# Kernel tuning notes

Measured on AMD Instinct MI355X. Metric: run time of the kernel, lower is better.

Reference implementation:

```python
import jax, jax.numpy as jnp
import numpy as np

BLOCK = 64  # quantization block size along in_features
IN, OUT, RANK, ALPHA = 4096, 4096, 16, 32
SCALING = ALPHA / RANK


def setup_inputs() -> dict:
    key = jax.random.key(0)
    ks = jax.random.split(key, 6)
    x = jax.random.normal(ks[0], (8, 1024, IN), dtype=jnp.float32)
    # int4 codes in [0, 15]; dequant subtracts 8 -> [-8, 7]
    qweight = jax.random.randint(ks[1], (OUT, IN), 0, 16, dtype=jnp.int32)
    # blockwise absmax-style scales, small positive
    scales = jax.random.uniform(ks[2], (OUT, IN // BLOCK), dtype=jnp.float32) * 0.02 + 1e-3
    bias = jax.random.normal(ks[3], (OUT,), dtype=jnp.float32) * 0.02
    lora_A = jax.random.normal(ks[4], (IN, RANK), dtype=jnp.float32) * 0.02
    lora_B = jnp.zeros((RANK, OUT), dtype=jnp.float32)
    return {"x": x, "qweight": qweight, "scales": scales, "bias": bias,
            "lora_A": lora_A, "lora_B": lora_B}


def _dequant(qweight, scales):
    # qweight: [out, in] int codes in [0,15]; scales: [out, in/BLOCK]
    out, in_f = qweight.shape
    q = (qweight.astype(jnp.float32) - 8.0).reshape(out, in_f // BLOCK, BLOCK)
    return (q * scales[:, :, None]).reshape(out, in_f)  # [out, in]


def reference(x, qweight, scales, bias, lora_A, lora_B):
    W = _dequant(qweight, scales)                      # [out, in]
    base = jnp.einsum('bsi,oi->bso', x, W) + bias      # quantized linear
    lora = jnp.einsum('bsr,ro->bso', jnp.einsum('bsi,ir->bsr', x, lora_A), lora_B)
    return base + lora * SCALING
```

## Files before the change

kernel.cpp:

```cpp
#include <hip/hip_runtime.h>
#include <hip/hip_bf16.h>

#define IN_F 4096
#define OUT_F 4096
#define M_TOK 8192
#define RANK 16

typedef __attribute__((ext_vector_type(4))) float f32x4;
typedef __attribute__((ext_vector_type(8))) short short8;

struct alignas(16) bf16x8_s { __hip_bfloat16 v[8]; };

#define CONV_BLOCKS 2048
#define CONV_ITERS (M_TOK * IN_F / (8 * 256 * CONV_BLOCKS))

__global__ __launch_bounds__(256) void conv_kernel(
    const float* __restrict__ x,
    __hip_bfloat16* __restrict__ xb) {
    size_t idx = (size_t)blockIdx.x * 256 + threadIdx.x;
    const size_t stride = (size_t)CONV_BLOCKS * 256;
#pragma unroll
    for (int it = 0; it < CONV_ITERS; ++it, idx += stride) {
        const size_t base = idx * 8;
        float4 v0 = *(const float4*)(x + base);
        float4 v1 = *(const float4*)(x + base + 4);
        bf16x8_s r;
        r.v[0] = __float2bfloat16(v0.x);
        r.v[1] = __float2bfloat16(v0.y);
        r.v[2] = __float2bfloat16(v0.z);
        r.v[3] = __float2bfloat16(v0.w);
        r.v[4] = __float2bfloat16(v1.x);
        r.v[5] = __float2bfloat16(v1.y);
        r.v[6] = __float2bfloat16(v1.z);
        r.v[7] = __float2bfloat16(v1.w);
        *(bf16x8_s*)(xb + base) = r;
    }
}

#define DEQ_BLOCKS 2048

__global__ __launch_bounds__(256) void deq_kernel(
    const int* __restrict__ q,
    const float* __restrict__ scales,
    const float* __restrict__ lA,
    const float* __restrict__ lB,
    __hip_bfloat16* __restrict__ W) {
    const int tid = threadIdx.x;
    const int bid = blockIdx.x;
    const int o0 = (bid >> 1) * 4;
    const int i0 = (bid & 1) * 2048 + tid * 8;

    float bw[16][4];
#pragma unroll
    for (int r = 0; r < 16; ++r)
#pragma unroll
        for (int oi = 0; oi < 4; ++oi)
            bw[r][oi] = 2.0f * lB[(size_t)r * OUT_F + o0 + oi];

    float fold[4][8];
#pragma unroll
    for (int e = 0; e < 8; ++e) {
        const float* ar = lA + (size_t)(i0 + e) * RANK;
        float4 a0 = *(const float4*)(ar + 0);
        float4 a1 = *(const float4*)(ar + 4);
        float4 a2 = *(const float4*)(ar + 8);
        float4 a3 = *(const float4*)(ar + 12);
#pragma unroll
        for (int oi = 0; oi < 4; ++oi) {
            float f = a0.x * bw[0][oi] + a0.y * bw[1][oi]
                    + a0.z * bw[2][oi] + a0.w * bw[3][oi]
                    + a1.x * bw[4][oi] + a1.y * bw[5][oi]
                    + a1.z * bw[6][oi] + a1.w * bw[7][oi]
                    + a2.x * bw[8][oi] + a2.y * bw[9][oi]
                    + a2.z * bw[10][oi] + a2.w * bw[11][oi]
                    + a3.x * bw[12][oi] + a3.y * bw[13][oi]
                    + a3.z * bw[14][oi] + a3.w * bw[15][oi];
            fold[oi][e] = f;
        }
    }

#pragma unroll
    for (int oi = 0; oi < 4; ++oi) {
        const int o = o0 + oi;
        const float s = scales[o * 64 + (i0 >> 6)];
        const int4* qp = (const int4*)(q + (size_t)o * IN_F + i0);
        int4 q0 = qp[0];
        int4 q1 = qp[1];
        bf16x8_s r;
        r.v[0] = __float2bfloat16(s * (float)(q0.x - 8) + fold[oi][0]);
        r.v[1] = __float2bfloat16(s * (float)(q0.y - 8) + fold[oi][1]);
        r.v[2] = __float2bfloat16(s * (float)(q0.z - 8) + fold[oi][2]);
        r.v[3] = __float2bfloat16(s * (float)(q0.w - 8) + fold[oi][3]);
        r.v[4] = __float2bfloat16(s * (float)(q1.x - 8) + fold[oi][4]);
        r.v[5] = __float2bfloat16(s * (float)(q1.y - 8) + fold[oi][5]);
        r.v[6] = __float2bfloat16(s * (float)(q1.z - 8) + fold[oi][6]);
        r.v[7] = __float2bfloat16(s * (float)(q1.w - 8) + fold[oi][7]);
        *(bf16x8_s*)(W + (size_t)o * IN_F + i0) = r;
    }
}

#define BK 64
#define NT (IN_F / BK)

__device__ __forceinline__ short8 ldfrag(const short* p, int half, int row, int gran) {
    return *(const short8*)(p + half * 8192 + row * 64 + ((gran ^ (row & 7)) * 8));
}

#define STAGE(LDSbuf, SRC, ROW0, K0)                                          \
    {                                                                         \
        _Pragma("unroll")                                                     \
        for (int j = 0; j < 2; ++j) {                                         \
            const __hip_bfloat16* g = (SRC) +                                 \
                (size_t)((ROW0) + j * 64 + wave * 8 + srow) * IN_F + (K0) + sgc; \
            __builtin_amdgcn_global_load_lds(                                 \
                (const __attribute__((address_space(1))) void*)g,             \
                (__attribute__((address_space(3))) void*)((LDSbuf) + (j * 64 + wave * 8) * 64), \
                16, 0, 0);                                                    \
        }                                                                     \
    }

#define PHASE(ABUF, BBUF, MH, KK, READB, STAGE_CODE, WAITCODE)                \
    {                                                                         \
        _Pragma("unroll") for (int f = 0; f < 4; ++f)                         \
            fa[f] = ldfrag(ABUF, MH, wm * 64 + f * 16 + fr, (KK) * 4 + fc);   \
        if (READB) {                                                          \
            _Pragma("unroll") for (int g2 = 0; g2 < 4; ++g2)                  \
                fb[g2] = ldfrag(BBUF, bhalf, brow0 + g2 * 16 + fr, (KK) * 4 + fc); \
        }                                                                     \
        STAGE_CODE;                                                           \
        WAITCODE;                                                             \
        __builtin_amdgcn_s_barrier();                                         \
        asm volatile("s_waitcnt lgkmcnt(0)" ::: "memory");                    \
        __builtin_amdgcn_sched_barrier(0);                                    \
        __builtin_amdgcn_s_setprio(1);                                        \
        _Pragma("unroll") for (int f = 0; f < 4; ++f)                         \
        _Pragma("unroll") for (int g2 = 0; g2 < 4; ++g2)                      \
            acc[(MH) * 4 + f][g2] =                                           \
                __builtin_amdgcn_mfma_f32_16x16x32_bf16(                      \
                    fa[f], fb[g2], acc[(MH) * 4 + f][g2], 0, 0, 0);           \
        __builtin_amdgcn_s_setprio(0);                                        \
        __builtin_amdgcn_s_barrier();                                         \
    }

__global__ __launch_bounds__(512, 2) void qlora_gemm_kernel(
    const __hip_bfloat16* __restrict__ xb,
    const __hip_bfloat16* __restrict__ Wq,
    const float* __restrict__ bias,
    float* __restrict__ out) {
    __shared__ __hip_bfloat16 As[2][16384];
    __shared__ __hip_bfloat16 Bs[2][16384];

    const int tid  = threadIdx.x;
    const int wave = tid >> 6;
    const int lane = tid & 63;
    const int wm = wave >> 2;
    const int wn = wave & 3;

    const int wg = ((int)blockIdx.x & 7) * 64 + ((int)blockIdx.x >> 3);
    const int bx = wg & 15;
    const int by = wg >> 4;
    const int m0 = by * 256;
    const int n0 = bx * 256;

    f32x4 acc[8][4];
#pragma unroll
    for (int i = 0; i < 8; ++i)
#pragma unroll
        for (int j = 0; j < 4; ++j)
            acc[i][j] = (f32x4){0.f, 0.f, 0.f, 0.f};

    const int srow = lane >> 3;
    const int sgc  = ((lane & 7) ^ srow) * 8;

    const int fr = lane & 15;
    const int fc = lane >> 4;

    const int bhalf = wn >> 1;
    const int brow0 = (wn & 1) * 64;

    const short* A0p = (const short*)As[0];
    const short* A1p = (const short*)As[1];
    const short* B0p = (const short*)Bs[0];
    const short* B1p = (const short*)Bs[1];

    short8 fa[4];
    short8 fb[4];

    STAGE(As[0],        xb, m0,       0);
    STAGE(Bs[0],        Wq, n0,       0);
    STAGE(As[0] + 8192, xb, m0 + 128, 0);
    STAGE(Bs[0] + 8192, Wq, n0 + 128, 0);
    STAGE(As[1],        xb, m0,       BK);
    STAGE(Bs[1],        Wq, n0,       BK);
    asm volatile("s_waitcnt vmcnt(4)" ::: "memory");
    __builtin_amdgcn_s_barrier();

    for (int it = 0; it < NT / 2; ++it) {
        const int t = it * 2;
        const int k_t1 = ((t + 1) & (NT - 1)) * BK;
        const int k_t2 = ((t + 2) & (NT - 1)) * BK;
        const int k_t3 = ((t + 3) & (NT - 1)) * BK;

        PHASE(A0p, B0p, 0, 0, 1, STAGE(As[1] + 8192, xb, m0 + 128, k_t1), );
        PHASE(A0p, B0p, 1, 0, 0, STAGE(Bs[1] + 8192, Wq, n0 + 128, k_t1), );
        PHASE(A0p, B0p, 0, 1, 1, , );
        PHASE(A0p, B0p, 1, 1, 0,
              { STAGE(As[0], xb, m0, k_t2); STAGE(Bs[0], Wq, n0, k_t2); },
              asm volatile("s_waitcnt vmcnt(4)" ::: "memory"));

        PHASE(A1p, B1p, 0, 0, 1, STAGE(As[0] + 8192, xb, m0 + 128, k_t2), );
        PHASE(A1p, B1p, 1, 0, 0, STAGE(Bs[0] + 8192, Wq, n0 + 128, k_t2), );
        PHASE(A1p, B1p, 0, 1, 1, , );
        PHASE(A1p, B1p, 1, 1, 0,
              { STAGE(As[1], xb, m0, k_t3); STAGE(Bs[1], Wq, n0, k_t3); },
              asm volatile("s_waitcnt vmcnt(4)" ::: "memory"));
    }

    asm volatile("s_waitcnt vmcnt(0)" ::: "memory");

    const int cc  = lane & 15;
    const int rr4 = (lane >> 4) * 4;
    float bv[4];
#pragma unroll
    for (int g2 = 0; g2 < 4; ++g2)
        bv[g2] = bias[n0 + wn * 64 + g2 * 16 + cc];

#pragma unroll
    for (int mh = 0; mh < 2; ++mh)
#pragma unroll
        for (int f = 0; f < 4; ++f) {
            const int m = m0 + mh * 128 + wm * 64 + f * 16 + rr4;
#pragma unroll
            for (int g2 = 0; g2 < 4; ++g2) {
                const int n = n0 + wn * 64 + g2 * 16 + cc;
                float* op = out + (size_t)m * OUT_F + n;
                const f32x4 a = acc[mh * 4 + f][g2];
#pragma unroll
                for (int r = 0; r < 4; ++r)
                    op[(size_t)r * OUT_F] = a[r] + bv[g2];
            }
        }
}

extern "C" void kernel_launch(void* const* d_in, const int* in_sizes, int n_in,
                              void* d_out, int out_size, void* d_ws, size_t ws_size,
                              hipStream_t stream) {
    const float* x      = (const float*)d_in[0];
    const int*   qw     = (const int*)  d_in[1];
    const float* scales = (const float*)d_in[2];
    const float* bias   = (const float*)d_in[3];
    const float* lA     = (const float*)d_in[4];
    const float* lB     = (const float*)d_in[5];
    float* out = (float*)d_out;

    char* ws = (char*)d_ws;
    __hip_bfloat16* Wq = (__hip_bfloat16*)ws;
    __hip_bfloat16* xb = (__hip_bfloat16*)(ws + (size_t)32 * 1024 * 1024);

    conv_kernel<<<CONV_BLOCKS, 256, 0, stream>>>(x, xb);
    deq_kernel<<<DEQ_BLOCKS, 256, 0, stream>>>(qw, scales, lA, lB, Wq);
    qlora_gemm_kernel<<<dim3(512), dim3(512), 0, stream>>>(xb, Wq, bias, out);
}
```

Measured before the change: 594.1 us.

## Double-buffer MFMA register fragments to overlap LDS reads with MFMA phases

Splits each phase so LDS fragment reads for the next phase are issued before the current phase's MFMAs, using two register sets (fa0/fa1, fb0/fb1) and partial lgkmcnt waits. The global-to-LDS stage schedule is also reshuffled, with the B second half for the next tile prefetched earlier. The aim is to hide LDS read latency behind matrix math, at the cost of more VGPRs and a fragile hand-tuned wait and stage ordering.

```diff
diff --git a/kernel.cpp b/kernel.cpp
--- a/kernel.cpp
+++ b/kernel.cpp
@@ -119,28 +119,25 @@
         }                                                                     \
     }
 
-#define PHASE(ABUF, BBUF, MH, KK, READB, STAGE_CODE, WAITCODE)                \
-    {                                                                         \
-        _Pragma("unroll") for (int f = 0; f < 4; ++f)                         \
-            fa[f] = ldfrag(ABUF, MH, wm * 64 + f * 16 + fr, (KK) * 4 + fc);   \
-        if (READB) {                                                          \
-            _Pragma("unroll") for (int g2 = 0; g2 < 4; ++g2)                  \
-                fb[g2] = ldfrag(BBUF, bhalf, brow0 + g2 * 16 + fr, (KK) * 4 + fc); \
-        }                                                                     \
-        STAGE_CODE;                                                           \
-        WAITCODE;                                                             \
-        __builtin_amdgcn_s_barrier();                                         \
-        asm volatile("s_waitcnt lgkmcnt(0)" ::: "memory");                    \
-        __builtin_amdgcn_sched_barrier(0);                                    \
-        __builtin_amdgcn_s_setprio(1);                                        \
-        _Pragma("unroll") for (int f = 0; f < 4; ++f)                         \
-        _Pragma("unroll") for (int g2 = 0; g2 < 4; ++g2)                      \
-            acc[(MH) * 4 + f][g2] =                                           \
-                __builtin_amdgcn_mfma_f32_16x16x32_bf16(                      \
-                    fa[f], fb[g2], acc[(MH) * 4 + f][g2], 0, 0, 0);           \
-        __builtin_amdgcn_s_setprio(0);                                        \
-        __builtin_amdgcn_s_barrier();                                         \
-    }
+#define RD_A(dst, BUF, HALF, KG)                                              \
+    _Pragma("unroll") for (int f = 0; f < 4; ++f)                             \
+        dst[f] = ldfrag(BUF, HALF, wm * 64 + f * 16 + fr, (KG) * 4 + fc);
+
+#define RD_B(dst, BUF, KG)                                                    \
+    _Pragma("unroll") for (int g2 = 0; g2 < 4; ++g2)                          \
+        dst[g2] = ldfrag(BUF, bhalf, brow0 + g2 * 16 + fr, (KG) * 4 + fc);
+
+#define PHASE_TAIL(LGK, FA, FB, AIDX)                                         \
+    __builtin_amdgcn_s_barrier();                                             \
+    asm volatile("s_waitcnt lgkmcnt(" #LGK ")" ::: "memory");                 \
+    __builtin_amdgcn_sched_barrier(0);                                        \
+    __builtin_amdgcn_s_setprio(1);                                            \
+    _Pragma("unroll") for (int f = 0; f < 4; ++f)                             \
+    _Pragma("unroll") for (int g2 = 0; g2 < 4; ++g2)                          \
+        acc[(AIDX) + f][g2] = __builtin_amdgcn_mfma_f32_16x16x32_bf16(        \
+            FA[f], FB[g2], acc[(AIDX) + f][g2], 0, 0, 0);                     \
+    __builtin_amdgcn_s_setprio(0);                                            \
+    __builtin_amdgcn_s_barrier();
 
 __global__ __launch_bounds__(512, 2) void qlora_gemm_kernel(
     const __hip_bfloat16* __restrict__ xb,
@@ -183,37 +180,54 @@
     const short* B0p = (const short*)Bs[0];
     const short* B1p = (const short*)Bs[1];
 
-    short8 fa[4];
-    short8 fb[4];
+    short8 fa0[4], fa1[4];
+    short8 fb0[4], fb1[4];
 
     STAGE(As[0],        xb, m0,       0);
+    STAGE(As[0] + 8192, xb, m0 + 128, 0);
     STAGE(Bs[0],        Wq, n0,       0);
-    STAGE(As[0] + 8192, xb, m0 + 128, 0);
     STAGE(Bs[0] + 8192, Wq, n0 + 128, 0);
     STAGE(As[1],        xb, m0,       BK);
     STAGE(Bs[1],        Wq, n0,       BK);
-    asm volatile("s_waitcnt vmcnt(4)" ::: "memory");
+    STAGE(Bs[1] + 8192, Wq, n0 + 128, BK);
+    asm volatile("s_waitcnt vmcnt(6)" ::: "memory");
     __builtin_amdgcn_s_barrier();
+    RD_A(fa0, A0p, 0, 0);
+    RD_B(fb0, B0p, 0);
 
     for (int it = 0; it < NT / 2; ++it) {
         const int t = it * 2;
-        const int k_t1 = ((t + 1) & (NT - 1)) * BK;
+        const int k_t1 = (t + 1) * BK;
         const int k_t2 = ((t + 2) & (NT - 1)) * BK;
         const int k_t3 = ((t + 3) & (NT - 1)) * BK;
 
-        PHASE(A0p, B0p, 0, 0, 1, STAGE(As[1] + 8192, xb, m0 + 128, k_t1), );
-        PHASE(A0p, B0p, 1, 0, 0, STAGE(Bs[1] + 8192, Wq, n0 + 128, k_t1), );
-        PHASE(A0p, B0p, 0, 1, 1, , );
-        PHASE(A0p, B0p, 1, 1, 0,
-              { STAGE(As[0], xb, m0, k_t2); STAGE(Bs[0], Wq, n0, k_t2); },
-              asm volatile("s_waitcnt vmcnt(4)" ::: "memory"));
-
-        PHASE(A1p, B1p, 0, 0, 1, STAGE(As[0] + 8192, xb, m0 + 128, k_t2), );
-        PHASE(A1p, B1p, 1, 0, 0, STAGE(Bs[0] + 8192, Wq, n0 + 128, k_t2), );
-        PHASE(A1p, B1p, 0, 1, 1, , );
-        PHASE(A1p, B1p, 1, 1, 0,
-              { STAGE(As[1], xb, m0, k_t3); STAGE(Bs[1], Wq, n0, k_t3); },
-              asm volatile("s_waitcnt vmcnt(4)" ::: "memory"));
+        RD_A(fa1, A0p, 0, 1); RD_B(fb1, B0p, 1);
+        STAGE(As[1] + 8192, xb, m0 + 128, k_t1);
+        PHASE_TAIL(8, fa0, fb0, 0)
+        RD_A(fa0, A0p, 1, 0);
+        PHASE_TAIL(4, fa1, fb1, 0)
+        RD_A(fa1, A0p, 1, 1);
+        STAGE(As[0], xb, m0, k_t2);
+        STAGE(Bs[0], Wq, n0, k_t2);
+        PHASE_TAIL(4, fa0, fb0, 4)
+        asm volatile("s_waitcnt vmcnt(4)" ::: "memory");
+        RD_A(fa0, A1p, 0, 0); RD_B(fb0, B1p, 0);
+        STAGE(Bs[0] + 8192, Wq, n0 + 128, k_t2);
+        PHASE_TAIL(8, fa1, fb1, 4)
+
+        RD_A(fa1, A1p, 0, 1); RD_B(fb1, B1p, 1);
+        STAGE(As[0] + 8192, xb, m0 + 128, k_t2);
+        PHASE_TAIL(8, fa0, fb0, 0)
+        RD_A(fa0, A1p, 1, 0);
+        PHASE_TAIL(4, fa1, fb1, 0)
+        RD_A(fa1, A1p, 1, 1);
+        STAGE(As[1], xb, m0, k_t3);
+        STAGE(Bs[1], Wq, n0, k_t3);
+        PHASE_TAIL(4, fa0, fb0, 4)
+        asm volatile("s_waitcnt vmcnt(4)" ::: "memory");
+        RD_A(fa0, A0p, 0, 0); RD_B(fb0, B0p, 0);
+        STAGE(Bs[1] + 8192, Wq, n0 + 128, k_t3);
+        PHASE_TAIL(8, fa1, fb1, 4)
     }
 
     asm volatile("s_waitcnt vmcnt(0)" ::: "memory");
```

New measurement: 608.5 us. 2.4% more time.

## Use one barrier per GEMM phase and split the GEMM into two launches

Applied to the files above, without the earlier changes.

Replaces the PHASE macro, which used two barriers, an explicit lgkmcnt wait, a sched_barrier and setprio, with a leaner sequence: one barrier per phase, then LDS fragment reads, async global-to-LDS staging and MFMAs. This is meant to cut synchronisation stalls and let the compiler overlap LDS reads with the matrix ops. The GEMM is also split into two 256-block launches, one per half of the token dimension, with the workgroup swizzle changed to match, probably to improve L2 locality. The risks are LDS read/write races now that the ordering is weaker, and lower occupancy, since each 256-block launch with two blocks per CU cannot fill the GPU.

```diff
diff --git a/kernel.cpp b/kernel.cpp
--- a/kernel.cpp
+++ b/kernel.cpp
@@ -119,28 +119,21 @@
         }                                                                     \
     }
 
-#define PHASE(ABUF, BBUF, MH, KK, READB, STAGE_CODE, WAITCODE)                \
-    {                                                                         \
-        _Pragma("unroll") for (int f = 0; f < 4; ++f)                         \
-            fa[f] = ldfrag(ABUF, MH, wm * 64 + f * 16 + fr, (KK) * 4 + fc);   \
-        if (READB) {                                                          \
-            _Pragma("unroll") for (int g2 = 0; g2 < 4; ++g2)                  \
-                fb[g2] = ldfrag(BBUF, bhalf, brow0 + g2 * 16 + fr, (KK) * 4 + fc); \
-        }                                                                     \
-        STAGE_CODE;                                                           \
-        WAITCODE;                                                             \
-        __builtin_amdgcn_s_barrier();                                         \
-        asm volatile("s_waitcnt lgkmcnt(0)" ::: "memory");                    \
-        __builtin_amdgcn_sched_barrier(0);                                    \
-        __builtin_amdgcn_s_setprio(1);                                        \
-        _Pragma("unroll") for (int f = 0; f < 4; ++f)                         \
-        _Pragma("unroll") for (int g2 = 0; g2 < 4; ++g2)                      \
-            acc[(MH) * 4 + f][g2] =                                           \
-                __builtin_amdgcn_mfma_f32_16x16x32_bf16(                      \
-                    fa[f], fb[g2], acc[(MH) * 4 + f][g2], 0, 0, 0);           \
-        __builtin_amdgcn_s_setprio(0);                                        \
-        __builtin_amdgcn_s_barrier();                                         \
-    }
+#define RD_A(BUF, HALF, KG)                                                   \
+    _Pragma("unroll") for (int f = 0; f < 4; ++f)                             \
+        fa[f] = ldfrag(BUF, HALF, wm * 64 + f * 16 + fr, (KG) * 4 + fc);
+
+#define RD_B(BUF, KG)                                                         \
+    _Pragma("unroll") for (int g2 = 0; g2 < 4; ++g2)                          \
+        fb[g2] = ldfrag(BUF, bhalf, brow0 + g2 * 16 + fr, (KG) * 4 + fc);
+
+#define MFMA16(MH)                                                            \
+    _Pragma("unroll") for (int f = 0; f < 4; ++f)                             \
+    _Pragma("unroll") for (int g2 = 0; g2 < 4; ++g2)                          \
+        acc[(MH) * 4 + f][g2] = __builtin_amdgcn_mfma_f32_16x16x32_bf16(      \
+            fa[f], fb[g2], acc[(MH) * 4 + f][g2], 0, 0, 0);
+
+#define BAR __builtin_amdgcn_s_barrier();
 
 __global__ __launch_bounds__(512, 2) void qlora_gemm_kernel(
     const __hip_bfloat16* __restrict__ xb,
@@ -156,7 +149,7 @@
     const int wm = wave >> 2;
     const int wn = wave & 3;
 
-    const int wg = ((int)blockIdx.x & 7) * 64 + ((int)blockIdx.x >> 3);
+    const int wg = ((int)blockIdx.x & 7) * 32 + ((int)blockIdx.x >> 3);
     const int bx = wg & 15;
     const int by = wg >> 4;
     const int m0 = by * 256;
@@ -187,33 +180,46 @@
     short8 fb[4];
 
     STAGE(As[0],        xb, m0,       0);
+    STAGE(As[0] + 8192, xb, m0 + 128, 0);
     STAGE(Bs[0],        Wq, n0,       0);
-    STAGE(As[0] + 8192, xb, m0 + 128, 0);
     STAGE(Bs[0] + 8192, Wq, n0 + 128, 0);
     STAGE(As[1],        xb, m0,       BK);
     STAGE(Bs[1],        Wq, n0,       BK);
     asm volatile("s_waitcnt vmcnt(4)" ::: "memory");
-    __builtin_amdgcn_s_barrier();
 
     for (int it = 0; it < NT / 2; ++it) {
         const int t = it * 2;
-        const int k_t1 = ((t + 1) & (NT - 1)) * BK;
+        const int k_t1 = (t + 1) * BK;
         const int k_t2 = ((t + 2) & (NT - 1)) * BK;
         const int k_t3 = ((t + 3) & (NT - 1)) * BK;
 
-        PHASE(A0p, B0p, 0, 0, 1, STAGE(As[1] + 8192, xb, m0 + 128, k_t1), );
-        PHASE(A0p, B0p, 1, 0, 0, STAGE(Bs[1] + 8192, Wq, n0 + 128, k_t1), );
-        PHASE(A0p, B0p, 0, 1, 1, , );
-        PHASE(A0p, B0p, 1, 1, 0,
-              { STAGE(As[0], xb, m0, k_t2); STAGE(Bs[0], Wq, n0, k_t2); },
-              asm volatile("s_waitcnt vmcnt(4)" ::: "memory"));
-
-        PHASE(A1p, B1p, 0, 0, 1, STAGE(As[0] + 8192, xb, m0 + 128, k_t2), );
-        PHASE(A1p, B1p, 1, 0, 0, STAGE(Bs[0] + 8192, Wq, n0 + 128, k_t2), );
-        PHASE(A1p, B1p, 0, 1, 1, , );
-        PHASE(A1p, B1p, 1, 1, 0,
-              { STAGE(As[1], xb, m0, k_t3); STAGE(Bs[1], Wq, n0, k_t3); },
-              asm volatile("s_waitcnt vmcnt(4)" ::: "memory"));
+        BAR RD_A(A0p, 0, 0) RD_B(B0p, 0)
+            STAGE(As[1] + 8192, xb, m0 + 128, k_t1)
+            MFMA16(0)
+        BAR RD_A(A0p, 1, 0)
+            STAGE(Bs[1] + 8192, Wq, n0 + 128, k_t1)
+            MFMA16(1)
+        BAR RD_A(A0p, 0, 1) RD_B(B0p, 1)
+            MFMA16(0)
+        BAR RD_A(A0p, 1, 1)
+            STAGE(As[0], xb, m0, k_t2)
+            STAGE(Bs[0], Wq, n0, k_t2)
+            MFMA16(1)
+        asm volatile("s_waitcnt vmcnt(4)" ::: "memory");
+
+        BAR RD_A(A1p, 0, 0) RD_B(B1p, 0)
+            STAGE(As[0] + 8192, xb, m0 + 128, k_t2)
+            MFMA16(0)
+        BAR RD_A(A1p, 1, 0)
+            STAGE(Bs[0] + 8192, Wq, n0 + 128, k_t2)
+            MFMA16(1)
+        BAR RD_A(A1p, 0, 1) RD_B(B1p, 1)
+            MFMA16(0)
+        BAR RD_A(A1p, 1, 1)
+            STAGE(As[1], xb, m0, k_t3)
+            STAGE(Bs[1], Wq, n0, k_t3)
+            MFMA16(1)
+        asm volatile("s_waitcnt vmcnt(4)" ::: "memory");
     }
 
     asm volatile("s_waitcnt vmcnt(0)" ::: "memory");
@@ -259,5 +265,8 @@
 
     conv_kernel<<<CONV_BLOCKS, 256, 0, stream>>>(x, xb);
     deq_kernel<<<DEQ_BLOCKS, 256, 0, stream>>>(qw, scales, lA, lB, Wq);
-    qlora_gemm_kernel<<<dim3(512), dim3(512), 0, stream>>>(xb, Wq, bias, out);
-}
+    const size_t half = (size_t)4096 * IN_F;
+    const size_t ohalf = (size_t)4096 * OUT_F;
+    qlora_gemm_kernel<<<dim3(256), dim3(512), 0, stream>>>(xb, Wq, bias, out);
+    qlora_gemm_kernel<<<dim3(256), dim3(512), 0, stream>>>(xb + half, Wq, bias, out + ohalf);
+}
```

Measured after the change: 582.0 us. 1.02x faster.
